# Kernel tuning notes

Hardware: AMD Instinct MI355X
Metric: run time of the kernel (lower is better)

## Reference

```python
import jax, jax.numpy as jnp
import numpy as np

NUM_EMBEDDINGS = 1024
EMBEDDING_DIM = 64
COMMITMENT_COST = 0.25
DECAY = 0.99
EPSILON = 1e-05
N_TOKENS = 131072


def setup_inputs() -> dict:
    key = jax.random.key(0)
    k1, k2, k3 = jax.random.split(key, 3)
    inputs = jax.random.normal(k1, (N_TOKENS, EMBEDDING_DIM), dtype=jnp.float32)
    embed_w = jax.random.normal(k2, (NUM_EMBEDDINGS, EMBEDDING_DIM), dtype=jnp.float32)
    ema_w = jax.random.normal(k3, (NUM_EMBEDDINGS, EMBEDDING_DIM), dtype=jnp.float32)
    ema_cluster_size = jnp.zeros((NUM_EMBEDDINGS,), dtype=jnp.float32)
    return {"inputs": inputs, "embed_w": embed_w, "ema_w": ema_w,
            "ema_cluster_size": ema_cluster_size}


def reference(inputs, embed_w, ema_w, ema_cluster_size):
    K = embed_w.shape[0]
    # squared L2 distances [N, K]
    distances = (jnp.sum(inputs ** 2, axis=1, keepdims=True)
                 + jnp.sum(embed_w ** 2, axis=1)
                 - 2.0 * inputs @ embed_w.T)
    encoding_indices = jnp.argmin(distances, axis=1)          # [N]
    encodings = jax.nn.one_hot(encoding_indices, K, dtype=inputs.dtype)  # [N, K]

    # EMA updates (training branch in the torch module)
    cluster_size = ema_cluster_size * DECAY + (1.0 - DECAY) * jnp.sum(encodings, axis=0)
    n = jnp.sum(cluster_size)
    cluster_size = (cluster_size + EPSILON) / (n + K * EPSILON) * n  # Laplace smoothing
    dw = jax.ops.segment_sum(inputs, encoding_indices, num_segments=K)  # == encodings.T @ inputs
    ema_w_new = ema_w * DECAY + (1.0 - DECAY) * dw
    embedding_new = ema_w_new / cluster_size[:, None]

    quantized = embedding_new[encoding_indices]               # == encodings @ embedding_new
    e_latent_loss = jnp.mean(0.5 * jnp.sum((jax.lax.stop_gradient(quantized) - inputs) ** 2, axis=1))
    loss = COMMITMENT_COST * e_latent_loss
    quantized = inputs + jax.lax.stop_gradient(quantized - inputs)  # straight-through

    avg_probs = jnp.mean(encodings, axis=0)
    perplexity = jnp.exp(-jnp.sum(avg_probs * jnp.log(avg_probs + 1e-10)))
    return (loss, quantized, perplexity, encodings)
```

## Files before the change

### kernel.cpp

```cpp
#include <hip/hip_runtime.h>

#define N_TOK 131072
#define KCODES 1024
#define DIM 64
#define QUANT_OFF 1
#define PERP_OFF 8388609
#define ENC_OFF ((size_t)8388610)

typedef __attribute__((ext_vector_type(8))) short short8v;
typedef __attribute__((ext_vector_type(4))) float f32x4;

__device__ __forceinline__ float wave_reduce_sum(float v) {
    #pragma unroll
    for (int o = 32; o > 0; o >>= 1) v += __shfl_xor(v, o, 64);
    return v;
}

__device__ __forceinline__ unsigned bf16_rne(float f) {
    unsigned u = __float_as_uint(f);
    return (u + 0x7FFFu + ((u >> 16) & 1u)) >> 16;
}

__device__ __forceinline__ void cvt8(const float4 a, const float4 b,
                                     short8v* h, short8v* l) {
    float f[8] = {a.x, a.y, a.z, a.w, b.x, b.y, b.z, b.w};
    #pragma unroll
    for (int j = 0; j < 8; ++j) {
        unsigned hb = bf16_rne(f[j]);
        float fh = __uint_as_float(hb << 16);
        unsigned lb = bf16_rne(f[j] - fh);
        (*h)[j] = (short)hb;
        (*l)[j] = (short)lb;
    }
}

__global__ void k0_prep(const float* __restrict__ ew, float* __restrict__ cbuf,
                        float* __restrict__ loss_acc, float* __restrict__ dwacc) {
    int tid = threadIdx.x;
    int lane = tid & 63;
    int wg = blockIdx.x * 4 + (tid >> 6);
    int gt = blockIdx.x * 256 + tid;
    if (gt == 0) *loss_acc = 0.0f;
    #pragma unroll
    for (int z = 0; z < 8; ++z) dwacc[gt * 8 + z] = 0.0f;
    #pragma unroll
    for (int k = 0; k < 8; ++k) {
        int row = wg * 8 + k;
        float v = ew[row * 64 + lane];
        float s = wave_reduce_sum(v * v);
        if (lane == 0) cbuf[row] = 0.5f * s;
    }
}

__global__ __launch_bounds__(256) void k1_argmin(
        const float* __restrict__ x, const float* __restrict__ ew,
        const float* __restrict__ cbuf, float* __restrict__ out,
        unsigned* __restrict__ idxbuf, unsigned* __restrict__ blockhist) {
    __shared__ unsigned short EH[128 * 64];
    __shared__ unsigned short EL[128 * 64];
    __shared__ float scc[128];
    __shared__ unsigned hist[1024];

    int tid = threadIdx.x;
    int lane = tid & 63;
    int wv = tid >> 6;
    int l15 = lane & 15;
    int l4 = lane >> 4;
    size_t t0 = (size_t)blockIdx.x * 256;
    size_t t0w = t0 + (size_t)wv * 64;

    #pragma unroll
    for (int q = 0; q < 4; ++q) hist[q * 256 + tid] = 0u;

    short8v ah[4][2], al[4][2];
    #pragma unroll
    for (int rt = 0; rt < 4; ++rt) {
        const float* xp = x + (t0w + rt * 16 + l15) * 64 + l4 * 8;
        #pragma unroll
        for (int s = 0; s < 2; ++s) {
            float4 a = *(const float4*)(xp + s * 32);
            float4 b = *(const float4*)(xp + s * 32 + 4);
            cvt8(a, b, &ah[rt][s], &al[rt][s]);
        }
    }

    float best[4][4];
    int bidx[4][4];
    #pragma unroll
    for (int rt = 0; rt < 4; ++rt)
        #pragma unroll
        for (int r = 0; r < 4; ++r) { best[rt][r] = -3.4e38f; bidx[rt][r] = 0; }

    for (int ch = 0; ch < 8; ++ch) {
        int c0 = ch * 128;
        {
            int r = tid >> 1, h = tid & 1;
            const float* ep = ew + (size_t)(c0 + r) * 64 + h * 32;
            #pragma unroll
            for (int q = 0; q < 4; ++q) {
                float4 a = *(const float4*)(ep + q * 8);
                float4 b = *(const float4*)(ep + q * 8 + 4);
                short8v hv, lv;
                cvt8(a, b, &hv, &lv);
                int byteoff = (r * 128 + h * 64 + q * 16) ^ ((r & 7) << 4);
                *(short8v*)((char*)EH + byteoff) = hv;
                *(short8v*)((char*)EL + byteoff) = lv;
            }
            if (tid < 128) scc[tid] = cbuf[c0 + tid];
        }
        __syncthreads();

        {
            float2 z; z.x = 0.0f; z.y = 0.0f;
            float* base = out + ENC_OFF + (t0 + (size_t)ch * 32) * 1024;
            #pragma unroll 4
            for (int u = 0; u < 64; ++u) {
                int idx = u * 256 + tid;
                int row = idx >> 9;
                int c2 = idx & 511;
                *(float2*)(base + (size_t)row * 1024 + c2 * 2) = z;
            }
        }

        #pragma unroll 2
        for (int ct = 0; ct < 8; ++ct) {
            int crow = ct * 16 + l15;
            int swz = (crow & 7) << 4;
            int b0 = (crow * 128 + l4 * 16) ^ swz;
            int b1 = (crow * 128 + 64 + l4 * 16) ^ swz;
            short8v bh0 = *(short8v*)((char*)EH + b0);
            short8v bl0 = *(short8v*)((char*)EL + b0);
            short8v bh1 = *(short8v*)((char*)EH + b1);
            short8v bl1 = *(short8v*)((char*)EL + b1);
            float sccv = scc[crow];
            int cid = c0 + crow;
            #pragma unroll
            for (int rt = 0; rt < 4; ++rt) {
                f32x4 acc = {0.f, 0.f, 0.f, 0.f};
                acc = __builtin_amdgcn_mfma_f32_16x16x32_bf16(ah[rt][0], bh0, acc, 0, 0, 0);
                acc = __builtin_amdgcn_mfma_f32_16x16x32_bf16(al[rt][0], bh0, acc, 0, 0, 0);
                acc = __builtin_amdgcn_mfma_f32_16x16x32_bf16(ah[rt][0], bl0, acc, 0, 0, 0);
                acc = __builtin_amdgcn_mfma_f32_16x16x32_bf16(al[rt][0], bl0, acc, 0, 0, 0);
                acc = __builtin_amdgcn_mfma_f32_16x16x32_bf16(ah[rt][1], bh1, acc, 0, 0, 0);
                acc = __builtin_amdgcn_mfma_f32_16x16x32_bf16(al[rt][1], bh1, acc, 0, 0, 0);
                acc = __builtin_amdgcn_mfma_f32_16x16x32_bf16(ah[rt][1], bl1, acc, 0, 0, 0);
                acc = __builtin_amdgcn_mfma_f32_16x16x32_bf16(al[rt][1], bl1, acc, 0, 0, 0);
                #pragma unroll
                for (int r = 0; r < 4; ++r) {
                    float sc = acc[r] - sccv;
                    if (sc > best[rt][r]) { best[rt][r] = sc; bidx[rt][r] = cid; }
                }
            }
        }
        __syncthreads();
    }

    #pragma unroll
    for (int rt = 0; rt < 4; ++rt)
        #pragma unroll
        for (int r = 0; r < 4; ++r) {
            float v = best[rt][r];
            int iv = bidx[rt][r];
            #pragma unroll
            for (int o = 1; o < 16; o <<= 1) {
                float vo = __shfl_xor(v, o, 64);
                int io = __shfl_xor(iv, o, 64);
                if (vo > v || (vo == v && io < iv)) { v = vo; iv = io; }
            }
            best[rt][r] = v;
            bidx[rt][r] = iv;
        }

    if (l15 == 0) {
        #pragma unroll
        for (int rt = 0; rt < 4; ++rt)
            #pragma unroll
            for (int r = 0; r < 4; ++r) {
                int bin = bidx[rt][r];
                unsigned rank = atomicAdd(&hist[bin], 1u);
                idxbuf[t0w + rt * 16 + l4 * 4 + r] = (unsigned)bin | (rank << 10);
            }
    }
    __syncthreads();
    #pragma unroll
    for (int q = 0; q < 4; ++q)
        blockhist[(size_t)blockIdx.x * 1024 + q * 256 + tid] = hist[q * 256 + tid];
}

__global__ void k2a_scan(const unsigned* __restrict__ blockhist,
                         unsigned* __restrict__ blockbase,
                         unsigned* __restrict__ counts) {
    int lane = threadIdx.x & 63;
    int bin = blockIdx.x * 4 + (threadIdx.x >> 6);
    unsigned v[8];
    unsigned s = 0;
    #pragma unroll
    for (int j = 0; j < 8; ++j) v[j] = blockhist[(size_t)(lane * 8 + j) * 1024 + bin];
    #pragma unroll
    for (int j = 0; j < 8; ++j) { unsigned t = v[j]; v[j] = s; s += t; }
    unsigned inc = s;
    for (int o = 1; o < 64; o <<= 1) {
        unsigned n = __shfl_up(inc, o, 64);
        if (lane >= o) inc += n;
    }
    unsigned excl = inc - s;
    #pragma unroll
    for (int j = 0; j < 8; ++j)
        blockbase[(size_t)(lane * 8 + j) * 1024 + bin] = excl + v[j];
    if (lane == 63) counts[bin] = inc;
}

__global__ void k2_stats(const float* __restrict__ ema_cs, const unsigned* __restrict__ counts,
                         float* __restrict__ smoothed, unsigned* __restrict__ offsets,
                         float* __restrict__ out) {
    __shared__ unsigned sc[1024];
    __shared__ float sf[1024];
    int t = threadIdx.x;
    unsigned cnt = counts[t];
    float cs = 0.99f * ema_cs[t] + 0.01f * (float)cnt;

    sf[t] = cs; __syncthreads();
    for (int o = 512; o > 0; o >>= 1) { if (t < o) sf[t] += sf[t + o]; __syncthreads(); }
    float n = sf[0];
    __syncthreads();
    smoothed[t] = (cs + 1e-5f) / (n + 1024.0f * 1e-5f) * n;

    sc[t] = cnt; __syncthreads();
    for (int o = 1; o < 1024; o <<= 1) {
        unsigned v = (t >= o) ? sc[t - o] : 0u;
        __syncthreads();
        sc[t] += v;
        __syncthreads();
    }
    offsets[t] = sc[t] - cnt;

    float p = (float)cnt / 131072.0f;
    sf[t] = p * logf(p + 1e-10f); __syncthreads();
    for (int o = 512; o > 0; o >>= 1) { if (t < o) sf[t] += sf[t + o]; __syncthreads(); }
    if (t == 0) out[PERP_OFF] = expf(-sf[0]);
}

__global__ void k3_scatter(const unsigned* __restrict__ idxbuf,
                           const unsigned* __restrict__ offsets,
                           const unsigned* __restrict__ blockbase,
                           int* __restrict__ toklist, int* __restrict__ clustid,
                           float* __restrict__ out) {
    int i = blockIdx.x * 256 + threadIdx.x;
    unsigned v = idxbuf[i];
    unsigned bin = v & 1023u;
    unsigned rank = v >> 10;
    unsigned pos = offsets[bin] + blockbase[(size_t)(i >> 8) * 1024 + bin] + rank;
    toklist[pos] = i;
    clustid[pos] = (int)bin;
    out[ENC_OFF + (size_t)i * 1024 + bin] = 1.0f;
}

__global__ void k4a_dw(const float* __restrict__ x, const int* __restrict__ toklist,
                       const int* __restrict__ clustid, float* __restrict__ dwacc) {
    int lane = threadIdx.x & 63, w = threadIdx.x >> 6;
    int p0 = blockIdx.x * 128 + w * 32;
    int cur = clustid[p0];
    float acc = 0.0f;
    #pragma unroll 4
    for (int t = 0; t < 32; ++t) {
        int pos = p0 + t;
        int c = clustid[pos];
        int tok = toklist[pos];
        float v = x[(size_t)tok * 64 + lane];
        if (c != cur) {
            atomicAdd(&dwacc[(size_t)cur * 64 + lane], acc);
            acc = 0.0f; cur = c;
        }
        acc += v;
    }
    atomicAdd(&dwacc[(size_t)cur * 64 + lane], acc);
}

__global__ void k4b_emb(const float* __restrict__ emaw, const float* __restrict__ dwacc,
                        const float* __restrict__ smoothed, float* __restrict__ embnew) {
    int t = blockIdx.x * 256 + threadIdx.x;
    int k = t >> 6;
    embnew[t] = (emaw[t] * 0.99f + 0.01f * dwacc[t]) / smoothed[k];
}

__global__ void k5_output(const float* __restrict__ x, const float* __restrict__ embnew,
                          const unsigned* __restrict__ idxbuf, float* __restrict__ out,
                          float* __restrict__ loss_acc) {
    int tid = threadIdx.x;
    int lane = tid & 63, w = tid >> 6;
    size_t wbase = ((size_t)blockIdx.x * 4 + w) * 32;
    int myidx = (int)(idxbuf[wbase + (lane & 31)] & 1023u);
    float ls = 0.0f;
    #pragma unroll 4
    for (int t = 0; t < 32; ++t) {
        size_t i = wbase + t;
        int ii = __shfl(myidx, t, 64);
        float q = embnew[(size_t)ii * 64 + lane];
        float xv = x[i * 64 + lane];
        out[QUANT_OFF + i * 64 + lane] = xv + (q - xv);
        float diff = q - xv;
        ls = fmaf(diff, diff, ls);
    }
    ls = wave_reduce_sum(ls);
    if (lane == 0) atomicAdd(loss_acc, ls);
}

__global__ void k6_loss(const float* __restrict__ loss_acc, float* __restrict__ out) {
    if (threadIdx.x == 0) out[0] = 0.25f * 0.5f * (*loss_acc) / 131072.0f;
}

extern "C" void kernel_launch(void* const* d_in, const int* in_sizes, int n_in,
                              void* d_out, int out_size, void* d_ws, size_t ws_size,
                              hipStream_t stream) {
    const float* x     = (const float*)d_in[0];
    const float* ew    = (const float*)d_in[1];
    const float* emaw  = (const float*)d_in[2];
    const float* emacs = (const float*)d_in[3];
    float* out = (float*)d_out;
    float* wsf = (float*)d_ws;

    float*    cbuf      = wsf;
    float*    smoothed  = wsf + 1024;
    unsigned* offsets   = (unsigned*)(wsf + 2048);
    unsigned* counts    = (unsigned*)(wsf + 3072);
    float*    loss_acc  = wsf + 4096;
    unsigned* idxbuf    = (unsigned*)(wsf + 4160);
    int*      toklist   = (int*)(wsf + 4160 + N_TOK);
    int*      clustid   = toklist + N_TOK;
    float*    dwacc     = wsf + 4160 + 3 * N_TOK;
    float*    embnew    = dwacc + 65536;
    unsigned* blockhist = (unsigned*)(embnew + 65536);
    unsigned* blockbase = blockhist + 512 * 1024;

    hipLaunchKernelGGL(k0_prep,   dim3(32),   dim3(256),  0, stream, ew, cbuf, loss_acc, dwacc);
    hipLaunchKernelGGL(k1_argmin, dim3(512),  dim3(256),  0, stream, x, ew, cbuf, out, idxbuf, blockhist);
    hipLaunchKernelGGL(k2a_scan,  dim3(256),  dim3(256),  0, stream, blockhist, blockbase, counts);
    hipLaunchKernelGGL(k2_stats,  dim3(1),    dim3(1024), 0, stream, emacs, counts, smoothed, offsets, out);
    hipLaunchKernelGGL(k3_scatter,dim3(512),  dim3(256),  0, stream, idxbuf, offsets, blockbase, toklist, clustid, out);
    hipLaunchKernelGGL(k4a_dw,    dim3(1024), dim3(256),  0, stream, x, toklist, clustid, dwacc);
    hipLaunchKernelGGL(k4b_emb,   dim3(256),  dim3(256),  0, stream, emaw, dwacc, smoothed, embnew);
    hipLaunchKernelGGL(k5_output, dim3(1024), dim3(256),  0, stream, x, embnew, idxbuf, out, loss_acc);
    hipLaunchKernelGGL(k6_loss,   dim3(1),    dim3(64),   0, stream, loss_acc, out);
}
```

Before: 716.7 us.

## Switch argmin to fp16 split MFMA with top-2 tracking and exact fp32 resolve

The distance GEMM now splits inputs into fp16 hi/lo pairs instead of bf16, and the codebook conversion moves into the prep kernel so each argmin block loads pre-split halves. Argmin blocks shrink to 128 tokens, and each token tracks its best two scores. Tokens whose top-2 gap falls below a threshold are queued and recomputed in exact fp32 by a new resolve kernel. The histogram moves into its own kernel, and the output and loss kernels are re-vectorized to use per-block partial sums instead of a global atomic. The cost is extra launches and a dependence on the suspect threshold for correctness; fp16 range could also be an issue for large values.

Result: slower. 734.2 us (+2.4%).

```diff
diff --git a/kernel.cpp b/kernel.cpp
--- a/kernel.cpp
+++ b/kernel.cpp
@@ -1,4 +1,5 @@
 #include <hip/hip_runtime.h>
+#include <hip/hip_fp16.h>
 
 #define N_TOK 131072
 #define KCODES 1024
@@ -6,8 +7,10 @@
 #define QUANT_OFF 1
 #define PERP_OFF 8388609
 #define ENC_OFF ((size_t)8388610)
-
-typedef __attribute__((ext_vector_type(8))) short short8v;
+#define EPS_SUSPECT 4e-3f
+
+typedef __attribute__((ext_vector_type(8))) unsigned short ushort8v;
+typedef __attribute__((ext_vector_type(8))) _Float16 half8v;
 typedef __attribute__((ext_vector_type(4))) float f32x4;
 
 __device__ __forceinline__ float wave_reduce_sum(float v) {
@@ -16,33 +19,41 @@
     return v;
 }
 
-__device__ __forceinline__ unsigned bf16_rne(float f) {
-    unsigned u = __float_as_uint(f);
-    return (u + 0x7FFFu + ((u >> 16) & 1u)) >> 16;
-}
-
-__device__ __forceinline__ void cvt8(const float4 a, const float4 b,
-                                     short8v* h, short8v* l) {
+__device__ __forceinline__ void cvt8h(const float4 a, const float4 b,
+                                      half8v* h, half8v* l) {
     float f[8] = {a.x, a.y, a.z, a.w, b.x, b.y, b.z, b.w};
     #pragma unroll
     for (int j = 0; j < 8; ++j) {
-        unsigned hb = bf16_rne(f[j]);
-        float fh = __uint_as_float(hb << 16);
-        unsigned lb = bf16_rne(f[j] - fh);
-        (*h)[j] = (short)hb;
-        (*l)[j] = (short)lb;
+        _Float16 hh = (_Float16)f[j];
+        float fh = (float)hh;
+        _Float16 ll = (_Float16)(f[j] - fh);
+        (*h)[j] = hh;
+        (*l)[j] = ll;
     }
 }
 
 __global__ void k0_prep(const float* __restrict__ ew, float* __restrict__ cbuf,
-                        float* __restrict__ loss_acc, float* __restrict__ dwacc) {
+                        unsigned short* __restrict__ ewh, unsigned short* __restrict__ ewl,
+                        float* __restrict__ dwacc, unsigned* __restrict__ suspcnt) {
     int tid = threadIdx.x;
     int lane = tid & 63;
     int wg = blockIdx.x * 4 + (tid >> 6);
     int gt = blockIdx.x * 256 + tid;
-    if (gt == 0) *loss_acc = 0.0f;
-    #pragma unroll
-    for (int z = 0; z < 8; ++z) dwacc[gt * 8 + z] = 0.0f;
+    if (gt == 0) *suspcnt = 0u;
+    #pragma unroll
+    for (int z = 0; z < 8; ++z) {
+        int e = gt * 8 + z;
+        float v = ew[e];
+        _Float16 hh = (_Float16)v;
+        float fh = (float)hh;
+        _Float16 ll = (_Float16)(v - fh);
+        unsigned short uh, ul;
+        __builtin_memcpy(&uh, &hh, 2);
+        __builtin_memcpy(&ul, &ll, 2);
+        ewh[e] = uh;
+        ewl[e] = ul;
+        dwacc[e] = 0.0f;
+    }
     #pragma unroll
     for (int k = 0; k < 8; ++k) {
         int row = wg * 8 + k;
@@ -53,58 +64,57 @@
 }
 
 __global__ __launch_bounds__(256) void k1_argmin(
-        const float* __restrict__ x, const float* __restrict__ ew,
-        const float* __restrict__ cbuf, float* __restrict__ out,
-        unsigned* __restrict__ idxbuf, unsigned* __restrict__ blockhist) {
+        const float* __restrict__ x, const unsigned short* __restrict__ ewh,
+        const unsigned short* __restrict__ ewl, const float* __restrict__ cbuf,
+        float* __restrict__ out, unsigned* __restrict__ idxbuf,
+        unsigned* __restrict__ susp, unsigned* __restrict__ suspcnt) {
     __shared__ unsigned short EH[128 * 64];
     __shared__ unsigned short EL[128 * 64];
     __shared__ float scc[128];
-    __shared__ unsigned hist[1024];
 
     int tid = threadIdx.x;
     int lane = tid & 63;
     int wv = tid >> 6;
     int l15 = lane & 15;
     int l4 = lane >> 4;
-    size_t t0 = (size_t)blockIdx.x * 256;
-    size_t t0w = t0 + (size_t)wv * 64;
-
-    #pragma unroll
-    for (int q = 0; q < 4; ++q) hist[q * 256 + tid] = 0u;
-
-    short8v ah[4][2], al[4][2];
-    #pragma unroll
-    for (int rt = 0; rt < 4; ++rt) {
+    size_t t0 = (size_t)blockIdx.x * 128;
+    size_t t0w = t0 + (size_t)wv * 32;
+
+    half8v ah[2][2], al[2][2];
+    #pragma unroll
+    for (int rt = 0; rt < 2; ++rt) {
         const float* xp = x + (t0w + rt * 16 + l15) * 64 + l4 * 8;
         #pragma unroll
         for (int s = 0; s < 2; ++s) {
             float4 a = *(const float4*)(xp + s * 32);
             float4 b = *(const float4*)(xp + s * 32 + 4);
-            cvt8(a, b, &ah[rt][s], &al[rt][s]);
-        }
-    }
-
-    float best[4][4];
-    int bidx[4][4];
-    #pragma unroll
-    for (int rt = 0; rt < 4; ++rt)
+            cvt8h(a, b, &ah[rt][s], &al[rt][s]);
+        }
+    }
+
+    float m1[2][4], m2[2][4];
+    int i1[2][4], i2[2][4];
+    #pragma unroll
+    for (int rt = 0; rt < 2; ++rt)
         #pragma unroll
-        for (int r = 0; r < 4; ++r) { best[rt][r] = -3.4e38f; bidx[rt][r] = 0; }
+        for (int r = 0; r < 4; ++r) {
+            m1[rt][r] = -3.4e38f; m2[rt][r] = -3.4e38f;
+            i1[rt][r] = 0; i2[rt][r] = 0;
+        }
 
     for (int ch = 0; ch < 8; ++ch) {
         int c0 = ch * 128;
         {
             int r = tid >> 1, h = tid & 1;
-            const float* ep = ew + (size_t)(c0 + r) * 64 + h * 32;
+            const unsigned short* gh = ewh + (size_t)(c0 + r) * 64 + h * 32;
+            const unsigned short* gl = ewl + (size_t)(c0 + r) * 64 + h * 32;
             #pragma unroll
             for (int q = 0; q < 4; ++q) {
-                float4 a = *(const float4*)(ep + q * 8);
-                float4 b = *(const float4*)(ep + q * 8 + 4);
-                short8v hv, lv;
-                cvt8(a, b, &hv, &lv);
+                ushort8v hv = *(const ushort8v*)(gh + q * 8);
+                ushort8v lv = *(const ushort8v*)(gl + q * 8);
                 int byteoff = (r * 128 + h * 64 + q * 16) ^ ((r & 7) << 4);
-                *(short8v*)((char*)EH + byteoff) = hv;
-                *(short8v*)((char*)EL + byteoff) = lv;
+                *(ushort8v*)((char*)EH + byteoff) = hv;
+                *(ushort8v*)((char*)EL + byteoff) = lv;
             }
             if (tid < 128) scc[tid] = cbuf[c0 + tid];
         }
@@ -112,9 +122,9 @@
 
         {
             float2 z; z.x = 0.0f; z.y = 0.0f;
-            float* base = out + ENC_OFF + (t0 + (size_t)ch * 32) * 1024;
+            float* base = out + ENC_OFF + (t0 + (size_t)ch * 16) * 1024;
             #pragma unroll 4
-            for (int u = 0; u < 64; ++u) {
+            for (int u = 0; u < 32; ++u) {
                 int idx = u * 256 + tid;
                 int row = idx >> 9;
                 int c2 = idx & 511;
@@ -128,27 +138,32 @@
             int swz = (crow & 7) << 4;
             int b0 = (crow * 128 + l4 * 16) ^ swz;
             int b1 = (crow * 128 + 64 + l4 * 16) ^ swz;
-            short8v bh0 = *(short8v*)((char*)EH + b0);
-            short8v bl0 = *(short8v*)((char*)EL + b0);
-            short8v bh1 = *(short8v*)((char*)EH + b1);
-            short8v bl1 = *(short8v*)((char*)EL + b1);
+            half8v bh0 = *(half8v*)((char*)EH + b0);
+            half8v bl0 = *(half8v*)((char*)EL + b0);
+            half8v bh1 = *(half8v*)((char*)EH + b1);
+            half8v bl1 = *(half8v*)((char*)EL + b1);
             float sccv = scc[crow];
             int cid = c0 + crow;
             #pragma unroll
-            for (int rt = 0; rt < 4; ++rt) {
+            for (int rt = 0; rt < 2; ++rt) {
                 f32x4 acc = {0.f, 0.f, 0.f, 0.f};
-                acc = __builtin_amdgcn_mfma_f32_16x16x32_bf16(ah[rt][0], bh0, acc, 0, 0, 0);
-                acc = __builtin_amdgcn_mfma_f32_16x16x32_bf16(al[rt][0], bh0, acc, 0, 0, 0);
-                acc = __builtin_amdgcn_mfma_f32_16x16x32_bf16(ah[rt][0], bl0, acc, 0, 0, 0);
-                acc = __builtin_amdgcn_mfma_f32_16x16x32_bf16(al[rt][0], bl0, acc, 0, 0, 0);
-                acc = __builtin_amdgcn_mfma_f32_16x16x32_bf16(ah[rt][1], bh1, acc, 0, 0, 0);
-                acc = __builtin_amdgcn_mfma_f32_16x16x32_bf16(al[rt][1], bh1, acc, 0, 0, 0);
-                acc = __builtin_amdgcn_mfma_f32_16x16x32_bf16(ah[rt][1], bl1, acc, 0, 0, 0);
-                acc = __builtin_amdgcn_mfma_f32_16x16x32_bf16(al[rt][1], bl1, acc, 0, 0, 0);
+                acc = __builtin_amdgcn_mfma_f32_16x16x32_f16(ah[rt][0], bh0, acc, 0, 0, 0);
+                acc = __builtin_amdgcn_mfma_f32_16x16x32_f16(al[rt][0], bh0, acc, 0, 0, 0);
+                acc = __builtin_amdgcn_mfma_f32_16x16x32_f16(ah[rt][0], bl0, acc, 0, 0, 0);
+                acc = __builtin_amdgcn_mfma_f32_16x16x32_f16(al[rt][0], bl0, acc, 0, 0, 0);
+                acc = __builtin_amdgcn_mfma_f32_16x16x32_f16(ah[rt][1], bh1, acc, 0, 0, 0);
+                acc = __builtin_amdgcn_mfma_f32_16x16x32_f16(al[rt][1], bh1, acc, 0, 0, 0);
+                acc = __builtin_amdgcn_mfma_f32_16x16x32_f16(ah[rt][1], bl1, acc, 0, 0, 0);
+                acc = __builtin_amdgcn_mfma_f32_16x16x32_f16(al[rt][1], bl1, acc, 0, 0, 0);
                 #pragma unroll
                 for (int r = 0; r < 4; ++r) {
                     float sc = acc[r] - sccv;
-                    if (sc > best[rt][r]) { best[rt][r] = sc; bidx[rt][r] = cid; }
+                    if (sc > m1[rt][r]) {
+                        m2[rt][r] = m1[rt][r]; i2[rt][r] = i1[rt][r];
+                        m1[rt][r] = sc; i1[rt][r] = cid;
+                    } else if (sc > m2[rt][r]) {
+                        m2[rt][r] = sc; i2[rt][r] = cid;
+                    }
                 }
             }
         }
@@ -156,30 +171,84 @@
     }
 
     #pragma unroll
-    for (int rt = 0; rt < 4; ++rt)
+    for (int rt = 0; rt < 2; ++rt)
         #pragma unroll
         for (int r = 0; r < 4; ++r) {
-            float v = best[rt][r];
-            int iv = bidx[rt][r];
+            float m1v = m1[rt][r], m2v = m2[rt][r];
+            int i1v = i1[rt][r], i2v = i2[rt][r];
             #pragma unroll
             for (int o = 1; o < 16; o <<= 1) {
-                float vo = __shfl_xor(v, o, 64);
-                int io = __shfl_xor(iv, o, 64);
-                if (vo > v || (vo == v && io < iv)) { v = vo; iv = io; }
-            }
-            best[rt][r] = v;
-            bidx[rt][r] = iv;
-        }
-
-    if (l15 == 0) {
+                float b1 = __shfl_xor(m1v, o, 64); int bi1 = __shfl_xor(i1v, o, 64);
+                float b2 = __shfl_xor(m2v, o, 64); int bi2 = __shfl_xor(i2v, o, 64);
+                if (b1 > m1v || (b1 == m1v && bi1 < i1v)) {
+                    float c2v; int c2i;
+                    if (m1v > b2 || (m1v == b2 && i1v < bi2)) { c2v = m1v; c2i = i1v; }
+                    else { c2v = b2; c2i = bi2; }
+                    m1v = b1; i1v = bi1; m2v = c2v; i2v = c2i;
+                } else {
+                    if (b1 > m2v || (b1 == m2v && bi1 < i2v)) { m2v = b1; i2v = bi1; }
+                }
+            }
+            if (l15 == 0) {
+                size_t tok = t0w + rt * 16 + l4 * 4 + r;
+                idxbuf[tok] = (unsigned)i1v;
+                if (m2v >= m1v - EPS_SUSPECT) {
+                    unsigned p = atomicAdd(suspcnt, 1u);
+                    susp[p] = (unsigned)tok;
+                }
+            }
+        }
+}
+
+__global__ void k1s_resolve(const float* __restrict__ x, const float* __restrict__ ew,
+                            const float* __restrict__ cbuf, const unsigned* __restrict__ susp,
+                            const unsigned* __restrict__ suspcnt, unsigned* __restrict__ idxbuf) {
+    int lane = threadIdx.x & 63;
+    int wid = blockIdx.x * 4 + (threadIdx.x >> 6);
+    unsigned n = *suspcnt;
+    for (unsigned s = wid; s < n; s += 256) {
+        unsigned tok = susp[s];
+        float4 xr[16];
+        const float4* xp = (const float4*)(x + (size_t)tok * 64);
         #pragma unroll
-        for (int rt = 0; rt < 4; ++rt)
+        for (int q = 0; q < 16; ++q) xr[q] = xp[q];
+        float best = -3.4e38f;
+        int bidx = 0;
+        for (int rr = 0; rr < 16; ++rr) {
+            int code = rr * 64 + lane;
+            const float4* ep = (const float4*)(ew + (size_t)code * 64);
+            float d = 0.0f;
             #pragma unroll
-            for (int r = 0; r < 4; ++r) {
-                int bin = bidx[rt][r];
-                unsigned rank = atomicAdd(&hist[bin], 1u);
-                idxbuf[t0w + rt * 16 + l4 * 4 + r] = (unsigned)bin | (rank << 10);
-            }
+            for (int q = 0; q < 16; ++q) {
+                float4 xv = xr[q];
+                float4 e = ep[q];
+                d = fmaf(xv.x, e.x, d); d = fmaf(xv.y, e.y, d);
+                d = fmaf(xv.z, e.z, d); d = fmaf(xv.w, e.w, d);
+            }
+            float sc = d - cbuf[code];
+            if (sc > best) { best = sc; bidx = code; }
+        }
+        #pragma unroll
+        for (int o = 1; o < 64; o <<= 1) {
+            float vo = __shfl_xor(best, o, 64);
+            int io = __shfl_xor(bidx, o, 64);
+            if (vo > best || (vo == best && io < bidx)) { best = vo; bidx = io; }
+        }
+        if (lane == 0) idxbuf[tok] = (unsigned)bidx;
+    }
+}
+
+__global__ void k1h_hist(unsigned* __restrict__ idxbuf, unsigned* __restrict__ blockhist) {
+    __shared__ unsigned hist[1024];
+    int tid = threadIdx.x;
+    #pragma unroll
+    for (int q = 0; q < 4; ++q) hist[q * 256 + tid] = 0u;
+    __syncthreads();
+    if (tid < 128) {
+        size_t tok = (size_t)blockIdx.x * 128 + tid;
+        unsigned bin = idxbuf[tok];
+        unsigned rank = atomicAdd(&hist[bin], 1u);
+        idxbuf[tok] = bin | (rank << 10);
     }
     __syncthreads();
     #pragma unroll
@@ -192,12 +261,12 @@
                          unsigned* __restrict__ counts) {
     int lane = threadIdx.x & 63;
     int bin = blockIdx.x * 4 + (threadIdx.x >> 6);
-    unsigned v[8];
+    unsigned v[16];
     unsigned s = 0;
     #pragma unroll
-    for (int j = 0; j < 8; ++j) v[j] = blockhist[(size_t)(lane * 8 + j) * 1024 + bin];
-    #pragma unroll
-    for (int j = 0; j < 8; ++j) { unsigned t = v[j]; v[j] = s; s += t; }
+    for (int j = 0; j < 16; ++j) v[j] = blockhist[(size_t)(lane * 16 + j) * 1024 + bin];
+    #pragma unroll
+    for (int j = 0; j < 16; ++j) { unsigned t = v[j]; v[j] = s; s += t; }
     unsigned inc = s;
     for (int o = 1; o < 64; o <<= 1) {
         unsigned n = __shfl_up(inc, o, 64);
@@ -205,8 +274,8 @@
     }
     unsigned excl = inc - s;
     #pragma unroll
-    for (int j = 0; j < 8; ++j)
-        blockbase[(size_t)(lane * 8 + j) * 1024 + bin] = excl + v[j];
+    for (int j = 0; j < 16; ++j)
+        blockbase[(size_t)(lane * 16 + j) * 1024 + bin] = excl + v[j];
     if (lane == 63) counts[bin] = inc;
 }
 
@@ -249,7 +318,7 @@
     unsigned v = idxbuf[i];
     unsigned bin = v & 1023u;
     unsigned rank = v >> 10;
-    unsigned pos = offsets[bin] + blockbase[(size_t)(i >> 8) * 1024 + bin] + rank;
+    unsigned pos = offsets[bin] + blockbase[(size_t)(i >> 7) * 1024 + bin] + rank;
     toklist[pos] = i;
     clustid[pos] = (int)bin;
     out[ENC_OFF + (size_t)i * 1024 + bin] = 1.0f;
@@ -285,28 +354,35 @@
 
 __global__ void k5_output(const float* __restrict__ x, const float* __restrict__ embnew,
                           const unsigned* __restrict__ idxbuf, float* __restrict__ out,
-                          float* __restrict__ loss_acc) {
+                          float* __restrict__ partials) {
+    __shared__ float red[4];
     int tid = threadIdx.x;
-    int lane = tid & 63, w = tid >> 6;
-    size_t wbase = ((size_t)blockIdx.x * 4 + w) * 32;
-    int myidx = (int)(idxbuf[wbase + (lane & 31)] & 1023u);
-    float ls = 0.0f;
-    #pragma unroll 4
-    for (int t = 0; t < 32; ++t) {
-        size_t i = wbase + t;
-        int ii = __shfl(myidx, t, 64);
-        float q = embnew[(size_t)ii * 64 + lane];
-        float xv = x[i * 64 + lane];
-        out[QUANT_OFF + i * 64 + lane] = xv + (q - xv);
-        float diff = q - xv;
-        ls = fmaf(diff, diff, ls);
-    }
+    int gid = blockIdx.x * 256 + tid;
+    size_t i = (size_t)(gid >> 4);
+    int c = (gid & 15) * 4;
+    unsigned ii = idxbuf[i] & 1023u;
+    float4 xv = *(const float4*)(x + i * 64 + c);
+    float4 q = *(const float4*)(embnew + (size_t)ii * 64 + c);
+    float* o = out + QUANT_OFF + i * 64 + c;
+    float d0 = q.x - xv.x, d1 = q.y - xv.y, d2 = q.z - xv.z, d3 = q.w - xv.w;
+    o[0] = xv.x + d0; o[1] = xv.y + d1; o[2] = xv.z + d2; o[3] = xv.w + d3;
+    float ls = d0 * d0 + d1 * d1 + d2 * d2 + d3 * d3;
     ls = wave_reduce_sum(ls);
-    if (lane == 0) atomicAdd(loss_acc, ls);
-}
-
-__global__ void k6_loss(const float* __restrict__ loss_acc, float* __restrict__ out) {
-    if (threadIdx.x == 0) out[0] = 0.25f * 0.5f * (*loss_acc) / 131072.0f;
+    if ((tid & 63) == 0) red[tid >> 6] = ls;
+    __syncthreads();
+    if (tid == 0) partials[blockIdx.x] = red[0] + red[1] + red[2] + red[3];
+}
+
+__global__ void k6_loss(const float* __restrict__ partials, float* __restrict__ out) {
+    __shared__ float red[4];
+    int tid = threadIdx.x;
+    float s = 0.0f;
+    #pragma unroll 8
+    for (int j = 0; j < 32; ++j) s += partials[tid + j * 256];
+    s = wave_reduce_sum(s);
+    if ((tid & 63) == 0) red[tid >> 6] = s;
+    __syncthreads();
+    if (tid == 0) out[0] = 0.125f * (red[0] + red[1] + red[2] + red[3]) / 131072.0f;
 }
 
 extern "C" void kernel_launch(void* const* d_in, const int* in_sizes, int n_in,
@@ -319,26 +395,32 @@
     float* out = (float*)d_out;
     float* wsf = (float*)d_ws;
 
-    float*    cbuf      = wsf;
-    float*    smoothed  = wsf + 1024;
-    unsigned* offsets   = (unsigned*)(wsf + 2048);
-    unsigned* counts    = (unsigned*)(wsf + 3072);
-    float*    loss_acc  = wsf + 4096;
-    unsigned* idxbuf    = (unsigned*)(wsf + 4160);
-    int*      toklist   = (int*)(wsf + 4160 + N_TOK);
-    int*      clustid   = toklist + N_TOK;
-    float*    dwacc     = wsf + 4160 + 3 * N_TOK;
-    float*    embnew    = dwacc + 65536;
-    unsigned* blockhist = (unsigned*)(embnew + 65536);
-    unsigned* blockbase = blockhist + 512 * 1024;
-
-    hipLaunchKernelGGL(k0_prep,   dim3(32),   dim3(256),  0, stream, ew, cbuf, loss_acc, dwacc);
-    hipLaunchKernelGGL(k1_argmin, dim3(512),  dim3(256),  0, stream, x, ew, cbuf, out, idxbuf, blockhist);
-    hipLaunchKernelGGL(k2a_scan,  dim3(256),  dim3(256),  0, stream, blockhist, blockbase, counts);
-    hipLaunchKernelGGL(k2_stats,  dim3(1),    dim3(1024), 0, stream, emacs, counts, smoothed, offsets, out);
-    hipLaunchKernelGGL(k3_scatter,dim3(512),  dim3(256),  0, stream, idxbuf, offsets, blockbase, toklist, clustid, out);
-    hipLaunchKernelGGL(k4a_dw,    dim3(1024), dim3(256),  0, stream, x, toklist, clustid, dwacc);
-    hipLaunchKernelGGL(k4b_emb,   dim3(256),  dim3(256),  0, stream, emaw, dwacc, smoothed, embnew);
-    hipLaunchKernelGGL(k5_output, dim3(1024), dim3(256),  0, stream, x, embnew, idxbuf, out, loss_acc);
-    hipLaunchKernelGGL(k6_loss,   dim3(1),    dim3(64),   0, stream, loss_acc, out);
-}
+    float*          cbuf      = wsf;
+    float*          smoothed  = wsf + 1024;
+    unsigned*       offsets   = (unsigned*)(wsf + 2048);
+    unsigned*       counts    = (unsigned*)(wsf + 3072);
+    float*          partials  = wsf + 4096;
+    unsigned*       suspcnt   = (unsigned*)(wsf + 12288);
+    unsigned*       idxbuf    = (unsigned*)(wsf + 12352);
+    unsigned*       susp      = idxbuf + N_TOK;
+    int*            toklist   = (int*)(susp + N_TOK);
+    int*            clustid   = toklist + N_TOK;
+    float*          dwacc     = wsf + 12352 + 4 * N_TOK;
+    float*          embnew    = dwacc + 65536;
+    unsigned*       blockhist = (unsigned*)(embnew + 65536);
+    unsigned*       blockbase = blockhist + 1024 * 1024;
+    unsigned short* ewh       = (unsigned short*)(blockbase + 1024 * 1024);
+    unsigned short* ewl       = ewh + 65536;
+
+    hipLaunchKernelGGL(k0_prep,    dim3(32),   dim3(256),  0, stream, ew, cbuf, ewh, ewl, dwacc, suspcnt);
+    hipLaunchKernelGGL(k1_argmin,  dim3(1024), dim3(256),  0, stream, x, ewh, ewl, cbuf, out, idxbuf, susp, suspcnt);
+    hipLaunchKernelGGL(k1s_resolve,dim3(64),   dim3(256),  0, stream, x, ew, cbuf, susp, suspcnt, idxbuf);
+    hipLaunchKernelGGL(k1h_hist,   dim3(1024), dim3(256),  0, stream, idxbuf, blockhist);
+    hipLaunchKernelGGL(k2a_scan,   dim3(256),  dim3(256),  0, stream, blockhist, blockbase, counts);
+    hipLaunchKernelGGL(k2_stats,   dim3(1),    dim3(1024), 0, stream, emacs, counts, smoothed, offsets, out);
+    hipLaunchKernelGGL(k3_scatter, dim3(512),  dim3(256),  0, stream, idxbuf, offsets, blockbase, toklist, clustid, out);
+    hipLaunchKernelGGL(k4a_dw,     dim3(1024), dim3(256),  0, stream, x, toklist, clustid, dwacc);
+    hipLaunchKernelGGL(k4b_emb,    dim3(256),  dim3(256),  0, stream, emaw, dwacc, smoothed, embnew);
+    hipLaunchKernelGGL(k5_output,  dim3(8192), dim3(256),  0, stream, x, embnew, idxbuf, out, partials);
+    hipLaunchKernelGGL(k6_loss,    dim3(1),    dim3(256),  0, stream, partials, out);
+}
```
